# Kernel tuning notes

Measured on AMD Instinct MI355X. Metric: run time of the kernel, lower is better.

Reference implementation:

```python
import jax, jax.numpy as jnp
import numpy as np

VOCAB, D_IN, D_H, N_REL, N_CLS = 10000, 256, 256, 3, 4
N_NODES, N_EDGES, N_GRAPHS = 100000, 300000, 512


def setup_inputs() -> dict:
    key = jax.random.key(0)
    ks = jax.random.split(key, 12)
    x = jax.random.randint(ks[0], (N_NODES,), 0, VOCAB)
    edge_index = jax.random.randint(ks[1], (2, N_EDGES), 0, N_NODES)
    edge_type = jax.random.randint(ks[2], (N_EDGES,), 0, N_REL)
    batch = jnp.sort(jax.random.randint(ks[3], (N_NODES,), 0, N_GRAPHS))
    s = 0.05
    embed_table = jax.random.normal(ks[4], (VOCAB, D_IN), jnp.float32) * s
    embed_table = embed_table.at[0].set(0.0)  # padding_idx=0
    W1 = jax.random.normal(ks[5], (N_REL, D_IN, D_H), jnp.float32) * s
    root1 = jax.random.normal(ks[6], (D_IN, D_H), jnp.float32) * s
    b1 = jnp.zeros((D_H,), jnp.float32)
    W2 = jax.random.normal(ks[7], (N_REL, D_H, D_H), jnp.float32) * s
    root2 = jax.random.normal(ks[8], (D_H, D_H), jnp.float32) * s
    b2 = jnp.zeros((D_H,), jnp.float32)
    lin_W = jax.random.normal(ks[9], (D_H, N_CLS), jnp.float32) * s
    lin_b = jnp.zeros((N_CLS,), jnp.float32)
    return {"x": x, "edge_index": edge_index, "edge_type": edge_type,
            "batch": batch, "num_graphs": N_GRAPHS,
            "embed_table": embed_table, "W1": W1, "root1": root1, "b1": b1,
            "W2": W2, "root2": root2, "b2": b2, "lin_W": lin_W, "lin_b": lin_b}


def rgcn_conv(h, W, root, b, src, dst, edge_type, n_nodes):
    # PyG RGCNConv: out = h @ root + b + sum_r mean_{edges of rel r into i}(h[src] @ W_r)
    out = h @ root + b
    for r in range(W.shape[0]):
        hr = h @ W[r]                                   # [N, d_out] dense GEMM
        mask = (edge_type == r)
        msg = jnp.where(mask[:, None], hr[src], 0.0)    # [E, d_out]
        agg = jax.ops.segment_sum(msg, dst, num_segments=n_nodes)
        cnt = jax.ops.segment_sum(mask.astype(h.dtype), dst, num_segments=n_nodes)
        out = out + agg / jnp.maximum(cnt, 1.0)[:, None]
    return out


def reference(x, edge_index, edge_type, batch, num_graphs,
              embed_table, W1, root1, b1, W2, root2, b2, lin_W, lin_b):
    n_nodes = x.shape[0]
    src, dst = edge_index[0], edge_index[1]
    h = embed_table[x]                                  # [N, D_IN]
    h = jax.nn.relu(rgcn_conv(h, W1, root1, b1, src, dst, edge_type, n_nodes))
    h = jax.nn.relu(rgcn_conv(h, W2, root2, b2, src, dst, edge_type, n_nodes))
    # global mean pool by graph id
    sums = jax.ops.segment_sum(h, batch, num_segments=num_graphs)
    cnts = jax.ops.segment_sum(jnp.ones((n_nodes,), h.dtype), batch, num_segments=num_graphs)
    g = sums / jnp.maximum(cnts, 1.0)[:, None]          # [G, D_H]
    return g @ lin_W + lin_b                            # [G, N_CLS]
```

## Files before the change

kernel.cpp:

```cpp
#include <hip/hip_runtime.h>

#define D 256
#define SB 1024
typedef __attribute__((ext_vector_type(8))) short short8;
typedef __attribute__((ext_vector_type(4))) float floatx4;

__device__ __forceinline__ unsigned short f2bf(float f) {
  unsigned int u = __float_as_uint(f);
  u = (u + 0x7FFF + ((u >> 16) & 1)) >> 16;
  return (unsigned short)u;
}
__device__ __forceinline__ float bf2f(unsigned short h) {
  return __uint_as_float(((unsigned int)h) << 16);
}

__device__ __forceinline__ void glds16(const void* g, void* l) {
  __builtin_amdgcn_global_load_lds(
      (const __attribute__((address_space(1))) unsigned int*)g,
      (__attribute__((address_space(3))) unsigned int*)l, 16, 0, 0);
}

__global__ __launch_bounds__(256) void k_setup(
    int* __restrict__ cur, int RN,
    const int* __restrict__ batch, int* __restrict__ gstart, int N, int G,
    const float* __restrict__ table, unsigned short* __restrict__ tableb, int TN,
    const float* __restrict__ root1, const float* __restrict__ W1,
    const float* __restrict__ root2, const float* __restrict__ W2,
    unsigned short* __restrict__ wb, int* __restrict__ zrowi,
    int g0, int g1, int g2, int g3) {
  int b = blockIdx.x, t = threadIdx.x;
  if (b < g0) {
    int i = b * 1024 + t * 4;
#pragma unroll
    for (int j = 0; j < 4; j++) if (i + j < RN) cur[i + j] = 0;
    if (b == 0 && t < 128) zrowi[t] = 0;
  } else if (b < g1) {
    int i = (b - g0) * 256 + t;
    if (i >= N) return;
    int bb = batch[i];
    if (i == 0) { for (int g = 0; g <= bb; g++) gstart[g] = 0; }
    else { int pb = batch[i - 1]; for (int g = pb + 1; g <= bb; g++) gstart[g] = i; }
    if (i == N - 1) { for (int g = bb + 1; g <= G; g++) gstart[g] = N; }
  } else if (b < g2) {
    int i = ((b - g1) * 256 + t) * 8;
    if (i < TN) {
      float4 f0 = *(const float4*)(table + i);
      float4 f1 = *(const float4*)(table + i + 4);
      ushort4 o0, o1;
      o0.x = f2bf(f0.x); o0.y = f2bf(f0.y); o0.z = f2bf(f0.z); o0.w = f2bf(f0.w);
      o1.x = f2bf(f1.x); o1.y = f2bf(f1.y); o1.z = f2bf(f1.z); o1.w = f2bf(f1.w);
      *(ushort4*)(tableb + i) = o0;
      *(ushort4*)(tableb + i + 4) = o1;
    }
  } else {
    int layer = (b < g3) ? 0 : 1;
    int idx = ((b - (layer ? g3 : g2)) * 256 + t);
    int mat = idx >> 16, rem = idx & 65535;
    int n = rem >> 8, k = rem & 255;
    const float* root = layer ? root2 : root1;
    const float* W = layer ? W2 : W1;
    const float* s = (mat == 0) ? root : (W + (size_t)(mat - 1) * 65536);
    wb[(size_t)layer * 4 * 65536 + idx] = f2bf(s[k * 256 + n]);
  }
}

__global__ __launch_bounds__(256) void k_count_i(const int* __restrict__ dst,
    const int* __restrict__ et, int* __restrict__ cnt, int E, int N) {
  int e = blockIdx.x * 256 + threadIdx.x;
  if (e >= E) return;
  atomicAdd(&cnt[et[e] * N + dst[e]], 1);
}

__global__ __launch_bounds__(256) void k_scan1(const int* __restrict__ in,
    int* __restrict__ bsum, int n) {
  __shared__ int s[256];
  int base = blockIdx.x * SB, t = threadIdx.x;
  int a = 0;
#pragma unroll
  for (int j = 0; j < 4; j++) { int i = base + t * 4 + j; if (i < n) a += in[i]; }
  s[t] = a; __syncthreads();
  for (int o = 128; o > 0; o >>= 1) { if (t < o) s[t] += s[t + o]; __syncthreads(); }
  if (t == 0) bsum[blockIdx.x] = s[0];
}

__global__ __launch_bounds__(256) void k_scan2(int* __restrict__ bsum, int nb,
    int* __restrict__ total_out) {
  __shared__ int s[256];
  int t = threadIdx.x;
  int v[4]; int a = 0;
#pragma unroll
  for (int j = 0; j < 4; j++) {
    int i = t * 4 + j;
    v[j] = (i < nb) ? bsum[i] : 0;
    a += v[j];
  }
  s[t] = a; __syncthreads();
  for (int o = 1; o < 256; o <<= 1) {
    int x_ = (t >= o) ? s[t - o] : 0;
    __syncthreads();
    s[t] += x_;
    __syncthreads();
  }
  int excl = (t > 0) ? s[t - 1] : 0;
#pragma unroll
  for (int j = 0; j < 4; j++) {
    int i = t * 4 + j;
    if (i < nb) { bsum[i] = excl; excl += v[j]; }
  }
  if (t == 255) *total_out = s[255];
}

__global__ __launch_bounds__(256) void k_scan3(const int* __restrict__ in,
    const int* __restrict__ bsum, int* __restrict__ off, int* __restrict__ cur,
    int n) {
  __shared__ int s[256];
  int base = blockIdx.x * SB, t = threadIdx.x;
  int v[4]; int a = 0;
#pragma unroll
  for (int j = 0; j < 4; j++) {
    int i = base + t * 4 + j;
    v[j] = (i < n) ? in[i] : 0;
    a += v[j];
  }
  s[t] = a; __syncthreads();
  for (int o = 1; o < 256; o <<= 1) {
    int x_ = (t >= o) ? s[t - o] : 0;
    __syncthreads();
    s[t] += x_;
    __syncthreads();
  }
  int excl = (t > 0 ? s[t - 1] : 0) + bsum[blockIdx.x];
#pragma unroll
  for (int j = 0; j < 4; j++) {
    int i = base + t * 4 + j;
    if (i < n) { off[i] = excl; cur[i] = excl; excl += v[j]; }
  }
}

__global__ __launch_bounds__(256) void k_place2(const int* __restrict__ src,
    const int* __restrict__ dst, const int* __restrict__ et,
    const int* __restrict__ x, int* __restrict__ cur,
    int* __restrict__ esx, int* __restrict__ ess, int E, int N) {
  int e = blockIdx.x * 256 + threadIdx.x;
  if (e >= E) return;
  int s = src[e];
  int pos = atomicAdd(&cur[et[e] * N + dst[e]], 1);
  esx[pos] = x[s];
  ess[pos] = s;
}

__global__ __launch_bounds__(256) void k_agg(const unsigned short* __restrict__ h,
    const int* __restrict__ rows, const int* __restrict__ off,
    unsigned short* __restrict__ out, int RN) {
  const int wave = threadIdx.x >> 6, lane = threadIdx.x & 63;
  const int base = (blockIdx.x * 4 + wave) * 8;
  if (base >= RN) return;

  int lo[8], hi[8];
#pragma unroll
  for (int j = 0; j < 8; j++) {
    int id = base + j;
    lo[j] = (id < RN) ? off[id] : 0;
    hi[j] = (id < RN) ? off[id + 1] : 0;
    if (hi[j] - lo[j] < 2) hi[j] = lo[j];
  }

  int r0[8];
#pragma unroll
  for (int j = 0; j < 8; j++)
    r0[j] = (hi[j] > lo[j]) ? rows[lo[j]] : 0;

  ushort4 v0[8];
#pragma unroll
  for (int j = 0; j < 8; j++)
    v0[j] = (hi[j] > lo[j])
        ? *(const ushort4*)(h + (size_t)r0[j] * D + lane * 4)
        : make_ushort4(0, 0, 0, 0);

  float a[8][4];
#pragma unroll
  for (int j = 0; j < 8; j++) {
    a[j][0] = bf2f(v0[j].x); a[j][1] = bf2f(v0[j].y);
    a[j][2] = bf2f(v0[j].z); a[j][3] = bf2f(v0[j].w);
  }

#pragma unroll
  for (int j = 0; j < 8; j++) {
    for (int p = lo[j] + 1; p < hi[j]; ++p) {
      int r = rows[p];
      ushort4 v = *(const ushort4*)(h + (size_t)r * D + lane * 4);
      a[j][0] += bf2f(v.x); a[j][1] += bf2f(v.y);
      a[j][2] += bf2f(v.z); a[j][3] += bf2f(v.w);
    }
  }

#pragma unroll
  for (int j = 0; j < 8; j++) {
    int id = base + j;
    if (id >= RN) continue;
    int c = hi[j] - lo[j];
    if (c < 2) continue;
    float inv = 1.0f / (float)c;
    ushort4 o;
    o.x = f2bf(a[j][0] * inv); o.y = f2bf(a[j][1] * inv);
    o.z = f2bf(a[j][2] * inv); o.w = f2bf(a[j][3] * inv);
    *(ushort4*)(out + (size_t)id * D + lane * 4) = o;
  }
}

__global__ __launch_bounds__(512) void k_lgemm(
    const unsigned short* __restrict__ Aroot, const int* __restrict__ gidx,
    const unsigned short* agg, const int* __restrict__ rows_,
    const int* __restrict__ off_, const unsigned short* __restrict__ zrow,
    const unsigned short* __restrict__ wb,
    const float* __restrict__ bias, unsigned short* Cout, int M, int N) {
  __shared__ unsigned short AsU[2][128 * 32];
  __shared__ unsigned short BsU[2][256 * 32];
  const int tid = threadIdx.x;
  const int w = tid >> 6, lane = tid & 63;
  const int wr = w >> 2, wc = w & 3;
  const int i0 = blockIdx.x * 128;
  const int ml = lane & 15, q = lane >> 4;

  const int arow = w * 16 + (lane >> 2);
  const int achunk = lane & 3;
  int ra = i0 + arow;
  int rac = (ra < M) ? ra : (M - 1);
  const int rowA0 = gidx ? gidx[rac] : rac;
  const unsigned short* abase[4];
  abase[0] = Aroot + (size_t)rowA0 * D + achunk * 8;
#pragma unroll
  for (int r = 0; r < 3; r++) {
    int id = r * N + rac;
    int lo = off_[id];
    int cnt = off_[id + 1] - lo;
    const unsigned short* b;
    if (cnt == 0) b = zrow;
    else if (cnt == 1) b = Aroot + (size_t)rows_[lo] * D;
    else b = agg + (size_t)id * D;
    abase[r + 1] = b + achunk * 8;
  }

  const int brow = w * 32 + (lane >> 2);
  const int bchunk = lane & 3;
  const size_t bofs = (size_t)brow * D + bchunk * 8;

  floatx4 acc[4][4];
#pragma unroll
  for (int i = 0; i < 4; i++)
#pragma unroll
    for (int j = 0; j < 4; j++) acc[i][j] = (floatx4){0.f, 0.f, 0.f, 0.f};

  unsigned short* aldst[2] = {&AsU[0][w * 512], &AsU[1][w * 512]};
  unsigned short* bldst0[2] = {&BsU[0][w * 1024], &BsU[1][w * 1024]};
  unsigned short* bldst1[2] = {&BsU[0][w * 1024 + 512], &BsU[1][w * 1024 + 512]};

  for (int step = 0; step < 16; ++step) {
    __syncthreads();
#pragma unroll
    for (int h = 0; h < 2; h++) {
      const int kabs = step * 64 + h * 32;
      const int seg = kabs >> 8, kloc = kabs & 255;
      glds16(abase[seg] + kloc, aldst[h]);
      const unsigned short* bb = wb + (size_t)seg * 65536 + bofs + kloc;
      glds16(bb, bldst0[h]);
      glds16(bb + 16 * D, bldst1[h]);
    }
    __syncthreads();

#pragma unroll
    for (int h = 0; h < 2; h++) {
      short8 aF[4], bF[4];
#pragma unroll
      for (int mi = 0; mi < 4; mi++)
        aF[mi] = *(const short8*)&AsU[h][(wr * 64 + mi * 16 + ml) * 32 + q * 8];
#pragma unroll
      for (int ni = 0; ni < 4; ni++)
        bF[ni] = *(const short8*)&BsU[h][(wc * 64 + ni * 16 + ml) * 32 + q * 8];
#pragma unroll
      for (int mi = 0; mi < 4; mi++)
#pragma unroll
        for (int ni = 0; ni < 4; ni++)
          acc[mi][ni] = __builtin_amdgcn_mfma_f32_16x16x32_bf16(
              aF[mi], bF[ni], acc[mi][ni], 0, 0, 0);
    }
  }

  __syncthreads();

  float bv[4];
#pragma unroll
  for (int ni = 0; ni < 4; ni++) bv[ni] = bias[wc * 64 + ni * 16 + ml];
#pragma unroll
  for (int mi = 0; mi < 4; mi++) {
#pragma unroll
    for (int ni = 0; ni < 4; ni++) {
      int col = wc * 64 + ni * 16 + ml;
#pragma unroll
      for (int j = 0; j < 4; j++) {
        int row = i0 + wr * 64 + mi * 16 + q * 4 + j;
        if (row < M) {
          float v = fmaxf(acc[mi][ni][j] + bv[ni], 0.f);
          Cout[(size_t)row * D + col] = f2bf(v);
        }
      }
    }
  }
}

__global__ __launch_bounds__(256) void k_poolfinal(
    const unsigned short* __restrict__ h, const int* __restrict__ gstart,
    const float* __restrict__ linW, const float* __restrict__ linb,
    float* __restrict__ out, int G) {
  __shared__ float red[4][D];
  __shared__ float sred[4][4];
  int g = blockIdx.x;
  int lo = gstart[g], hi = gstart[g + 1];
  int tid = threadIdx.x, wave = tid >> 6, lane = tid & 63;
  float a0 = 0.f, a1 = 0.f, a2 = 0.f, a3 = 0.f;
  for (int i = lo + wave; i < hi; i += 4) {
    ushort4 v = *(const ushort4*)(h + (size_t)i * D + lane * 4);
    a0 += bf2f(v.x); a1 += bf2f(v.y); a2 += bf2f(v.z); a3 += bf2f(v.w);
  }
  red[wave][lane * 4 + 0] = a0;
  red[wave][lane * 4 + 1] = a1;
  red[wave][lane * 4 + 2] = a2;
  red[wave][lane * 4 + 3] = a3;
  __syncthreads();
  float s = red[0][tid] + red[1][tid] + red[2][tid] + red[3][tid];
  float inv = (hi > lo) ? 1.0f / (float)(hi - lo) : 0.0f;
  float m = s * inv;
  float4 wrow = *(const float4*)(linW + tid * 4);
  float p0 = m * wrow.x, p1 = m * wrow.y, p2 = m * wrow.z, p3 = m * wrow.w;
  for (int o = 32; o > 0; o >>= 1) {
    p0 += __shfl_down(p0, o, 64);
    p1 += __shfl_down(p1, o, 64);
    p2 += __shfl_down(p2, o, 64);
    p3 += __shfl_down(p3, o, 64);
  }
  if (lane == 0) {
    sred[wave][0] = p0; sred[wave][1] = p1;
    sred[wave][2] = p2; sred[wave][3] = p3;
  }
  __syncthreads();
  if (tid < 4)
    out[g * 4 + tid] = sred[0][tid] + sred[1][tid] + sred[2][tid] +
                       sred[3][tid] + linb[tid];
}

extern "C" void kernel_launch(void* const* d_in, const int* in_sizes, int n_in,
                              void* d_out, int out_size, void* d_ws, size_t ws_size,
                              hipStream_t stream) {
  const int*   x     = (const int*)d_in[0];
  const int*   ei    = (const int*)d_in[1];
  const int*   et    = (const int*)d_in[2];
  const int*   batch = (const int*)d_in[3];
  const float* table = (const float*)d_in[5];
  const float* W1    = (const float*)d_in[6];
  const float* root1 = (const float*)d_in[7];
  const float* b1    = (const float*)d_in[8];
  const float* W2    = (const float*)d_in[9];
  const float* root2 = (const float*)d_in[10];
  const float* b2    = (const float*)d_in[11];
  const float* linW  = (const float*)d_in[12];
  const float* linb  = (const float*)d_in[13];
  float* out = (float*)d_out;

  const int N = in_sizes[0];
  const int E = in_sizes[2];
  const int G = out_size / 4;
  const int VOC = in_sizes[5] / D;
  const int* src = ei;
  const int* dst = ei + E;
  const int RN = 3 * N;

  char* wsb = (char*)d_ws;
  size_t pg = (size_t)N * D * 2;
  unsigned short* P0 = (unsigned short*)wsb;
  unsigned short* P1 = (unsigned short*)(wsb + pg);
  unsigned short* P3 = (unsigned short*)(wsb + 3 * pg);
  unsigned short* wb = (unsigned short*)(wsb + 4 * pg);
  unsigned short* zrow = wb + 2 * 4 * 65536;
  int*   off    = (int*)(zrow + 256);
  int*   esx    = off + (RN + 1);
  int*   ess    = esx + E;
  int*   gstart = ess + E;
  unsigned short* tableb = P3;
  int* cur  = (int*)P0;
  int* bsum = cur + RN;

  const int nb = (RN + SB - 1) / SB;

  int nbZero = (RN + 1023) / 1024;
  int nbBounds = (N + 255) / 256;
  int nbCvt = (VOC * D / 8 + 255) / 256;
  int g0 = nbZero, g1 = g0 + nbBounds, g2 = g1 + nbCvt, g3 = g2 + 1024;
  k_setup<<<g3 + 1024, 256, 0, stream>>>(cur, RN, batch, gstart, N, G,
      table, tableb, VOC * D, root1, W1, root2, W2, wb, (int*)zrow,
      g0, g1, g2, g3);

  k_count_i<<<(E + 255) / 256, 256, 0, stream>>>(dst, et, cur, E, N);
  k_scan1<<<nb, 256, 0, stream>>>(cur, bsum, RN);
  k_scan2<<<1, 256, 0, stream>>>(bsum, nb, off + RN);
  k_scan3<<<nb, 256, 0, stream>>>(cur, bsum, off, cur, RN);
  k_place2<<<(E + 255) / 256, 256, 0, stream>>>(src, dst, et, x, cur, esx, ess, E, N);

  const int gagg = (RN + 31) / 32;
  const int ggemm = (N + 127) / 128;

  k_agg<<<gagg, 256, 0, stream>>>(tableb, esx, off, P0, RN);
  k_lgemm<<<ggemm, 512, 0, stream>>>(tableb, x, P0, esx, off, zrow, wb, b1, P0, N, N);
  k_agg<<<gagg, 256, 0, stream>>>(P0, ess, off, P1, RN);
  k_lgemm<<<ggemm, 512, 0, stream>>>(P0, nullptr, P1, ess, off, zrow,
                                     wb + 4 * 65536, b2, P1, N, N);

  k_poolfinal<<<G, 256, 0, stream>>>(P1, gstart, linW, linb, out, G);
}
```

Baseline: 375.5 us.

## Precompute layer-1 transforms over vocabulary and gather transformed rows per node

Layer 1 input is an embedding lookup, so the root and per-relation weight products are computed once over the 10000-row vocabulary table (4 small GEMMs) instead of over 100000 nodes. A new combine kernel then gathers the transformed rows by token id for the self term and by source token for each relation's mean aggregation, adds the bias and applies ReLU. This replaces the layer-1 aggregation pass and the large node-level GEMM with a much smaller GEMM plus gathers. The cost is an extra bf16 rounding of the transformed rows before they are averaged, and the gathers read from a 4x vocabulary-sized buffer.

```diff
diff --git a/kernel.cpp b/kernel.cpp
--- a/kernel.cpp
+++ b/kernel.cpp
@@ -208,6 +208,155 @@
   }
 }
 
+__global__ __launch_bounds__(512) void k_tgemm(
+    const unsigned short* __restrict__ tableb,
+    const unsigned short* __restrict__ wb1,
+    unsigned short* __restrict__ T, int VOCN, int nbm) {
+  __shared__ unsigned short AsU[2][128 * 32];
+  __shared__ unsigned short BsU[2][256 * 32];
+  const int tid = threadIdx.x;
+  const int w = tid >> 6, lane = tid & 63;
+  const int wr = w >> 2, wc = w & 3;
+  const int mat = blockIdx.x / nbm;
+  const int i0 = (blockIdx.x % nbm) * 128;
+  const int ml = lane & 15, q = lane >> 4;
+
+  const int arow = w * 16 + (lane >> 2);
+  const int achunk = lane & 3;
+  int ra = i0 + arow;
+  int rac = (ra < VOCN) ? ra : (VOCN - 1);
+  const unsigned short* abase = tableb + (size_t)rac * D + achunk * 8;
+
+  const int brow = w * 32 + (lane >> 2);
+  const int bchunk = lane & 3;
+  const unsigned short* bbase = wb1 + (size_t)mat * 65536
+                              + (size_t)brow * D + bchunk * 8;
+
+  floatx4 acc[4][4];
+#pragma unroll
+  for (int i = 0; i < 4; i++)
+#pragma unroll
+    for (int j = 0; j < 4; j++) acc[i][j] = (floatx4){0.f, 0.f, 0.f, 0.f};
+
+  unsigned short* aldst[2] = {&AsU[0][w * 512], &AsU[1][w * 512]};
+  unsigned short* bldst0[2] = {&BsU[0][w * 1024], &BsU[1][w * 1024]};
+  unsigned short* bldst1[2] = {&BsU[0][w * 1024 + 512], &BsU[1][w * 1024 + 512]};
+
+  for (int step = 0; step < 4; ++step) {
+    __syncthreads();
+#pragma unroll
+    for (int h = 0; h < 2; h++) {
+      const int kloc = step * 64 + h * 32;
+      glds16(abase + kloc, aldst[h]);
+      glds16(bbase + kloc, bldst0[h]);
+      glds16(bbase + 16 * D + kloc, bldst1[h]);
+    }
+    __syncthreads();
+
+#pragma unroll
+    for (int h = 0; h < 2; h++) {
+      short8 aF[4], bF[4];
+#pragma unroll
+      for (int mi = 0; mi < 4; mi++)
+        aF[mi] = *(const short8*)&AsU[h][(wr * 64 + mi * 16 + ml) * 32 + q * 8];
+#pragma unroll
+      for (int ni = 0; ni < 4; ni++)
+        bF[ni] = *(const short8*)&BsU[h][(wc * 64 + ni * 16 + ml) * 32 + q * 8];
+#pragma unroll
+      for (int mi = 0; mi < 4; mi++)
+#pragma unroll
+        for (int ni = 0; ni < 4; ni++)
+          acc[mi][ni] = __builtin_amdgcn_mfma_f32_16x16x32_bf16(
+              aF[mi], bF[ni], acc[mi][ni], 0, 0, 0);
+    }
+  }
+
+#pragma unroll
+  for (int mi = 0; mi < 4; mi++) {
+#pragma unroll
+    for (int ni = 0; ni < 4; ni++) {
+      int col = wc * 64 + ni * 16 + ml;
+#pragma unroll
+      for (int j = 0; j < 4; j++) {
+        int row = i0 + wr * 64 + mi * 16 + q * 4 + j;
+        if (row < VOCN)
+          T[((size_t)mat * VOCN + row) * D + col] = f2bf(acc[mi][ni][j]);
+      }
+    }
+  }
+}
+
+__global__ __launch_bounds__(256) void k_combine(
+    const int* __restrict__ x, const int* __restrict__ esx,
+    const int* __restrict__ off, const unsigned short* __restrict__ T,
+    const float* __restrict__ bias, unsigned short* __restrict__ outP,
+    int N, int VOCN) {
+  const int wave = threadIdx.x >> 6, lane = threadIdx.x & 63;
+  const int base = (blockIdx.x * 4 + wave) * 8;
+  if (base >= N) return;
+  float4 bv = *(const float4*)(bias + lane * 4);
+
+  float a[8][4];
+#pragma unroll
+  for (int j = 0; j < 8; j++) {
+    int id = base + j;
+    int xr = (id < N) ? x[id] : 0;
+    ushort4 v = *(const ushort4*)(T + (size_t)xr * D + lane * 4);
+    a[j][0] = bf2f(v.x) + bv.x; a[j][1] = bf2f(v.y) + bv.y;
+    a[j][2] = bf2f(v.z) + bv.z; a[j][3] = bf2f(v.w) + bv.w;
+  }
+
+  for (int r = 0; r < 3; ++r) {
+    const unsigned short* Tr = T + (size_t)(r + 1) * VOCN * D;
+    int lo[8], hi[8];
+#pragma unroll
+    for (int j = 0; j < 8; j++) {
+      int id = base + j;
+      lo[j] = (id < N) ? off[r * N + id] : 0;
+      hi[j] = (id < N) ? off[r * N + id + 1] : 0;
+    }
+    ushort4 v0[8];
+#pragma unroll
+    for (int j = 0; j < 8; j++)
+      v0[j] = (hi[j] > lo[j])
+          ? *(const ushort4*)(Tr + (size_t)esx[lo[j]] * D + lane * 4)
+          : make_ushort4(0, 0, 0, 0);
+    float s[8][4];
+#pragma unroll
+    for (int j = 0; j < 8; j++) {
+      s[j][0] = bf2f(v0[j].x); s[j][1] = bf2f(v0[j].y);
+      s[j][2] = bf2f(v0[j].z); s[j][3] = bf2f(v0[j].w);
+    }
+#pragma unroll
+    for (int j = 0; j < 8; j++) {
+      for (int p = lo[j] + 1; p < hi[j]; ++p) {
+        ushort4 v = *(const ushort4*)(Tr + (size_t)esx[p] * D + lane * 4);
+        s[j][0] += bf2f(v.x); s[j][1] += bf2f(v.y);
+        s[j][2] += bf2f(v.z); s[j][3] += bf2f(v.w);
+      }
+    }
+#pragma unroll
+    for (int j = 0; j < 8; j++) {
+      int c = hi[j] - lo[j];
+      if (c > 0) {
+        float inv = 1.0f / (float)c;
+        a[j][0] += s[j][0] * inv; a[j][1] += s[j][1] * inv;
+        a[j][2] += s[j][2] * inv; a[j][3] += s[j][3] * inv;
+      }
+    }
+  }
+
+#pragma unroll
+  for (int j = 0; j < 8; j++) {
+    int id = base + j;
+    if (id >= N) continue;
+    ushort4 o;
+    o.x = f2bf(fmaxf(a[j][0], 0.f)); o.y = f2bf(fmaxf(a[j][1], 0.f));
+    o.z = f2bf(fmaxf(a[j][2], 0.f)); o.w = f2bf(fmaxf(a[j][3], 0.f));
+    *(ushort4*)(outP + (size_t)id * D + lane * 4) = o;
+  }
+}
+
 __global__ __launch_bounds__(512) void k_lgemm(
     const unsigned short* __restrict__ Aroot, const int* __restrict__ gidx,
     const unsigned short* agg, const int* __restrict__ rows_,
@@ -386,6 +535,7 @@
   int*   ess    = esx + E;
   int*   gstart = ess + E;
   unsigned short* tableb = P3;
+  unsigned short* Tbuf = P1;
   int* cur  = (int*)P0;
   int* bsum = cur + RN;
 
@@ -405,11 +555,13 @@
   k_scan3<<<nb, 256, 0, stream>>>(cur, bsum, off, cur, RN);
   k_place2<<<(E + 255) / 256, 256, 0, stream>>>(src, dst, et, x, cur, esx, ess, E, N);
 
+  const int nbm = (VOC + 127) / 128;
+  k_tgemm<<<nbm * 4, 512, 0, stream>>>(tableb, wb, Tbuf, VOC, nbm);
+  k_combine<<<(N + 31) / 32, 256, 0, stream>>>(x, esx, off, Tbuf, b1, P0, N, VOC);
+
   const int gagg = (RN + 31) / 32;
   const int ggemm = (N + 127) / 128;
 
-  k_agg<<<gagg, 256, 0, stream>>>(tableb, esx, off, P0, RN);
-  k_lgemm<<<ggemm, 512, 0, stream>>>(tableb, x, P0, esx, off, zrow, wb, b1, P0, N, N);
   k_agg<<<gagg, 256, 0, stream>>>(P0, ess, off, P1, RN);
   k_lgemm<<<ggemm, 512, 0, stream>>>(P0, nullptr, P1, ess, off, zrow,
                                      wb + 4 * 65536, b2, P1, N, N);
```

Measured after the change: 524.6 us. 1.4x slower.
